# Kernel tuning notes

Hardware: AMD Instinct MI355X
Metric: run time of the kernel (lower is better)

Reference implementation:

```python
import jax, jax.numpy as jnp
import numpy as np

N_NODES = 50000
N_FEAT = 32
HIDDEN = 64
K_HOPS = 3
N_EDGES = 800000
BN_EPS = 1e-5


def setup_inputs() -> dict:
    key = jax.random.key(0)
    ks = jax.random.split(key, 16)
    x = jax.random.normal(ks[0], (N_NODES, N_FEAT), jnp.float32)
    edge_index = jax.random.randint(ks[1], (2, N_EDGES), 0, N_NODES, jnp.int32)
    edge_weight = jax.random.uniform(ks[2], (N_EDGES,), jnp.float32, minval=0.1, maxval=1.0)
    fin = N_FEAT + HIDDEN  # DCRNN cell concatenates [X, H]
    s = 1.0 / np.sqrt(fin)
    Wz = jax.random.uniform(ks[3], (2, K_HOPS, fin, HIDDEN), jnp.float32, -s, s)
    Wr = jax.random.uniform(ks[4], (2, K_HOPS, fin, HIDDEN), jnp.float32, -s, s)
    Wh = jax.random.uniform(ks[5], (2, K_HOPS, fin, HIDDEN), jnp.float32, -s, s)
    bz = jax.random.uniform(ks[6], (HIDDEN,), jnp.float32, -s, s)
    br = jax.random.uniform(ks[7], (HIDDEN,), jnp.float32, -s, s)
    bh = jax.random.uniform(ks[8], (HIDDEN,), jnp.float32, -s, s)
    g = 1.0 / np.sqrt(HIDDEN)
    gcn_w = jax.random.uniform(ks[9], (HIDDEN, HIDDEN), jnp.float32, -g, g)
    gcn_b = jax.random.uniform(ks[10], (HIDDEN,), jnp.float32, -g, g)
    bn_gamma = jnp.ones((HIDDEN,), jnp.float32)
    bn_beta = jnp.zeros((HIDDEN,), jnp.float32)
    lin_w = jax.random.uniform(ks[11], (HIDDEN, 1), jnp.float32, -g, g)
    lin_b = jax.random.uniform(ks[12], (1,), jnp.float32, -g, g)
    return dict(x=x, edge_index=edge_index, edge_weight=edge_weight,
                Wz=Wz, bz=bz, Wr=Wr, br=br, Wh=Wh, bh=bh,
                gcn_w=gcn_w, gcn_b=gcn_b, bn_gamma=bn_gamma, bn_beta=bn_beta,
                lin_w=lin_w, lin_b=lin_b)


def _dconv(X, W, b, row, col, ew, do_inv, di_inv, n):
    # Diffusion conv: H = sum_k T_out^k(X) @ W[0,k] + T_in^k(X) @ W[1,k] + b
    # T_out: propagate along edges (source -> target), out-degree normalized
    # T_in : propagate along reversed edges, in-degree normalized
    H = X @ W[0, 0] + X @ W[1, 0]
    Tx_o = X
    Tx_i = X
    w_out = (ew * do_inv[row])[:, None]  # [E,1]
    w_in = (ew * di_inv[col])[:, None]   # [E,1]
    for k in range(1, W.shape[1]):
        Tx_o = jax.ops.segment_sum(w_out * Tx_o[row], col, num_segments=n)
        Tx_i = jax.ops.segment_sum(w_in * Tx_i[col], row, num_segments=n)
        H = H + Tx_o @ W[0, k] + Tx_i @ W[1, k]
    return H + b


def reference(x, edge_index, edge_weight, Wz, bz, Wr, br, Wh, bh,
              gcn_w, gcn_b, bn_gamma, bn_beta, lin_w, lin_b):
    n = x.shape[0]
    row, col = edge_index[0], edge_index[1]
    # weighted degrees (as in DConv's dense-adjacency degree computation)
    deg_out = jax.ops.segment_sum(edge_weight, row, num_segments=n)
    deg_in = jax.ops.segment_sum(edge_weight, col, num_segments=n)
    do_inv = jnp.where(deg_out > 0, 1.0 / deg_out, 0.0)
    di_inv = jnp.where(deg_in > 0, 1.0 / deg_in, 0.0)

    # --- DCRNN cell (GRU with diffusion convs), hidden state starts at zero ---
    H0 = jnp.zeros((n, Wz.shape[-1]), x.dtype)
    XH = jnp.concatenate([x, H0], axis=1)
    Z = jax.nn.sigmoid(_dconv(XH, Wz, bz, row, col, edge_weight, do_inv, di_inv, n))
    R = jax.nn.sigmoid(_dconv(XH, Wr, br, row, col, edge_weight, do_inv, di_inv, n))
    XHR = jnp.concatenate([x, H0 * R], axis=1)
    H_tilde = jnp.tanh(_dconv(XHR, Wh, bh, row, col, edge_weight, do_inv, di_inv, n))
    H = Z * H0 + (1.0 - Z) * H_tilde  # [N, HIDDEN]

    # --- GCNConv(H, edge_index) with unit edge weights + self loops, sym norm ---
    xw = H @ gcn_w
    ones_e = jnp.ones((row.shape[0],), x.dtype)
    deg = jax.ops.segment_sum(ones_e, col, num_segments=n) + 1.0  # + self loop
    dis = jnp.where(deg > 0, jax.lax.rsqrt(deg), 0.0)
    norm = (dis[row] * dis[col])[:, None]
    y = jax.ops.segment_sum(norm * xw[row], col, num_segments=n) + (dis * dis)[:, None] * xw
    y = y + gcn_b

    # ReLU -> BatchNorm1d (batch statistics, biased var) -> Dropout(identity/eval) -> Linear
    y = jax.nn.relu(y)
    mean = jnp.mean(y, axis=0)
    var = jnp.mean(jnp.square(y - mean), axis=0)
    y = (y - mean) * jax.lax.rsqrt(var + BN_EPS) * bn_gamma + bn_beta
    out = y @ lin_w + lin_b  # [N, 1]
    return out
```

## Files before the change

### kernel.cpp

```cpp
#include <hip/hip_runtime.h>
#include <hip/hip_fp16.h>
#include <math.h>


#define BN_EPS 1e-5f
#define CAPB 6
#define CAP  64
#define ITEMS 2048
#define KI 8
#define REGCAP 5120

typedef _Float16 v8h __attribute__((ext_vector_type(8)));
typedef float v4f __attribute__((ext_vector_type(4)));

__global__ __launch_bounds__(256) void k_sort1(
    const int* __restrict__ row, const int* __restrict__ col,
    const float* __restrict__ ew,
    unsigned long long* __restrict__ bufC, unsigned long long* __restrict__ bufR,
    unsigned* __restrict__ gcnt, int E, int nbk, int reg) {
    __shared__ unsigned hist[256], scanb[256], cur[256], runb[256];
    __shared__ unsigned long long outb[ITEMS];
    int t = threadIdx.x;
    int s = (blockIdx.x >= nbk) ? 1 : 0;
    int blk = blockIdx.x - s * nbk;
    int e0 = blk * ITEMS;
    int vcnt = E - e0; if (vcnt > ITEMS) vcnt = ITEMS;
    hist[t] = 0;
    __syncthreads();
    for (int k = 0; k < KI; ++k) {
        int e = e0 + k * 256 + t;
        if (e < E) {
            int key = s ? row[e] : col[e];
            atomicAdd(&hist[key >> 8], 1u);
        }
    }
    __syncthreads();
    scanb[t] = hist[t];
    __syncthreads();
    for (int off = 1; off < 256; off <<= 1) {
        unsigned v = (t >= off) ? scanb[t - off] : 0u;
        __syncthreads();
        scanb[t] += v;
        __syncthreads();
    }
    unsigned excl = scanb[t] - hist[t];
    __syncthreads();
    scanb[t] = excl;
    cur[t] = excl;
    runb[t] = (unsigned)(t * reg) + atomicAdd(&gcnt[s * 256 + t], hist[t]);
    __syncthreads();
    for (int k = 0; k < KI; ++k) {
        int e = e0 + k * 256 + t;
        if (e < E) {
            int key, oth;
            if (s) { key = row[e]; oth = col[e]; }
            else   { key = col[e]; oth = row[e]; }
            unsigned hw = (unsigned)__half_as_ushort(__float2half(ew[e]));
            unsigned long long it = ((unsigned long long)(unsigned)key << 32)
                                  | ((unsigned)oth << 16) | hw;
            unsigned r = atomicAdd(&cur[key >> 8], 1u);
            outb[r] = it;
        }
    }
    __syncthreads();
    unsigned long long* buf = s ? bufR : bufC;
    for (int k = 0; k < KI; ++k) {
        int idx = k * 256 + t;
        if (idx < vcnt) {
            unsigned long long it = outb[idx];
            unsigned d = (unsigned)(it >> 40) & 255u;
            buf[(size_t)runb[d] + ((unsigned)idx - scanb[d])] = it;
        }
    }
}

__device__ inline float ent_w(unsigned e) {
    return __half2float(__ushort_as_half((unsigned short)(e & 0xffffu)));
}

__global__ __launch_bounds__(256) void k_sort2(
    const unsigned long long* __restrict__ bufC, const unsigned long long* __restrict__ bufR,
    const unsigned* __restrict__ gcnt,
    unsigned* __restrict__ ent_col, unsigned* __restrict__ ent_row,
    int* __restrict__ cnt_col, int* __restrict__ cnt_row,
    float* __restrict__ di_inv, float* __restrict__ do_inv, float* __restrict__ dis,
    int N, int reg, int ndig) {
    __shared__ unsigned hist[256], scanb[256], cur[256];
    __shared__ unsigned outp[REGCAP];
    __shared__ unsigned char outl[REGCAP];
    int t = threadIdx.x;
    int s = (blockIdx.x >= ndig) ? 1 : 0;
    int d0 = blockIdx.x - s * ndig;
    const unsigned long long* src = (s ? bufR : bufC) + (size_t)d0 * reg;
    unsigned* ent = s ? ent_row : ent_col;
    int cin = (int)gcnt[s * 256 + d0]; if (cin > REGCAP) cin = REGCAP;
    hist[t] = 0;
    __syncthreads();
    for (int i = t; i < cin; i += 256) {
        unsigned l = (unsigned)(src[i] >> 32) & 255u;
        atomicAdd(&hist[l], 1u);
    }
    __syncthreads();
    scanb[t] = hist[t];
    __syncthreads();
    for (int off = 1; off < 256; off <<= 1) {
        unsigned v = (t >= off) ? scanb[t - off] : 0u;
        __syncthreads();
        scanb[t] += v;
        __syncthreads();
    }
    unsigned excl = scanb[t] - hist[t];
    __syncthreads();
    scanb[t] = excl;
    cur[t] = excl;
    __syncthreads();
    for (int i = t; i < cin; i += 256) {
        unsigned long long it = src[i];
        unsigned l = (unsigned)(it >> 32) & 255u;
        unsigned r = atomicAdd(&cur[l], 1u);
        outp[r] = (unsigned)it;
        outl[r] = (unsigned char)l;
    }
    __syncthreads();
    int node0 = d0 << 8;
    for (int i = t; i < cin; i += 256) {
        unsigned l = outl[i];
        int slot = i - (int)scanb[l];
        int node = node0 + (int)l;
        if (slot < CAP && node < N)
            ent[((size_t)node << CAPB) + slot] = outp[i];
    }
    int node = node0 + t;
    if (node < N) {
        unsigned beg = scanb[t], n = hist[t];
        float sum = 0.f;
        for (unsigned j = 0; j < n; ++j) sum += ent_w(outp[beg + j]);
        float inv = sum > 0.f ? 1.f / sum : 0.f;
        if (s) { do_inv[node] = inv; cnt_row[node] = (int)n; }
        else   { di_inv[node] = inv; cnt_col[node] = (int)n;
                 dis[node] = rsqrtf((float)n + 1.0f); }
    }
}

__global__ void k_cvt_x(const float* __restrict__ xf, __half* __restrict__ xh, int n2) {
    int t = blockIdx.x * blockDim.x + threadIdx.x;
    if (t >= n2) return;
    float2 v = *(const float2*)(xf + 2 * (size_t)t);
    __half2 h; h.x = __float2half(v.x); h.y = __float2half(v.y);
    *(__half2*)(xh + 2 * (size_t)t) = h;
}

__global__ void k_hop(const unsigned* __restrict__ ent_col, const unsigned* __restrict__ ent_row,
                      const int* __restrict__ cnt_col, const int* __restrict__ cnt_row,
                      const __half* __restrict__ So, const __half* __restrict__ Si,
                      const float* __restrict__ do_inv, const float* __restrict__ di_inv,
                      __half* __restrict__ Do, __half* __restrict__ Di, int N) {
    int t = blockIdx.x * blockDim.x + threadIdx.x;
    int f = t & 31;
    int p = t >> 5;
    if (p >= 2 * N) return;
    const unsigned* ent; const __half* S; const float* inv; __half* D;
    int d, cnt;
    if (p < N) { d = p;     ent = ent_col; S = So; inv = do_inv; D = Do; cnt = min(cnt_col[d], CAP); }
    else       { d = p - N; ent = ent_row; S = Si; inv = di_inv; D = Di; cnt = min(cnt_row[d], CAP); }
    ent += ((size_t)d << CAPB);
    float acc = 0.f;
    int j = 0;
    for (; j + 7 < cnt; j += 8) {
        unsigned e0 = ent[j],     e1 = ent[j + 1], e2 = ent[j + 2], e3 = ent[j + 3];
        unsigned e4 = ent[j + 4], e5 = ent[j + 5], e6 = ent[j + 6], e7 = ent[j + 7];
        int s0 = e0 >> 16, s1 = e1 >> 16, s2 = e2 >> 16, s3 = e3 >> 16;
        int s4 = e4 >> 16, s5 = e5 >> 16, s6 = e6 >> 16, s7 = e7 >> 16;
        float i0 = inv[s0], i1 = inv[s1], i2 = inv[s2], i3 = inv[s3];
        float i4 = inv[s4], i5 = inv[s5], i6 = inv[s6], i7 = inv[s7];
        float v0 = __half2float(S[(size_t)s0 * 32 + f]);
        float v1 = __half2float(S[(size_t)s1 * 32 + f]);
        float v2 = __half2float(S[(size_t)s2 * 32 + f]);
        float v3 = __half2float(S[(size_t)s3 * 32 + f]);
        float v4 = __half2float(S[(size_t)s4 * 32 + f]);
        float v5 = __half2float(S[(size_t)s5 * 32 + f]);
        float v6 = __half2float(S[(size_t)s6 * 32 + f]);
        float v7 = __half2float(S[(size_t)s7 * 32 + f]);
        acc += ent_w(e0) * i0 * v0 + ent_w(e1) * i1 * v1
             + ent_w(e2) * i2 * v2 + ent_w(e3) * i3 * v3
             + ent_w(e4) * i4 * v4 + ent_w(e5) * i5 * v5
             + ent_w(e6) * i6 * v6 + ent_w(e7) * i7 * v7;
    }
    for (; j + 3 < cnt; j += 4) {
        unsigned e0 = ent[j],     e1 = ent[j + 1];
        unsigned e2 = ent[j + 2], e3 = ent[j + 3];
        int s0 = e0 >> 16, s1 = e1 >> 16, s2 = e2 >> 16, s3 = e3 >> 16;
        float i0 = inv[s0], i1 = inv[s1], i2 = inv[s2], i3 = inv[s3];
        float v0 = __half2float(S[(size_t)s0 * 32 + f]);
        float v1 = __half2float(S[(size_t)s1 * 32 + f]);
        float v2 = __half2float(S[(size_t)s2 * 32 + f]);
        float v3 = __half2float(S[(size_t)s3 * 32 + f]);
        acc += ent_w(e0) * i0 * v0 + ent_w(e1) * i1 * v1
             + ent_w(e2) * i2 * v2 + ent_w(e3) * i3 * v3;
    }
    for (; j < cnt; ++j) {
        unsigned e0 = ent[j];
        int s0 = e0 >> 16;
        acc += ent_w(e0) * inv[s0] * __half2float(S[(size_t)s0 * 32 + f]);
    }
    D[(size_t)d * 32 + f] = __float2half(acc);
}

__global__ void k_wprep(const float* __restrict__ Wz, const float* __restrict__ Wh,
                        const float* __restrict__ gcn_w,
                        __half* __restrict__ wzT, __half* __restrict__ whT,
                        __half* __restrict__ gwT) {
    int t = blockIdx.x * blockDim.x + threadIdx.x;
    if (t < 64 * 160) {
        int c = t / 160, k = t % 160;
        int blk = k >> 5, r = k & 31;
        float vz, vh;
        if (blk == 0) {
            vz = Wz[r * 64 + c] + Wz[(288 + r) * 64 + c];
            vh = Wh[r * 64 + c] + Wh[(288 + r) * 64 + c];
        } else {
            int kk = (blk + 1) >> 1, dd = (blk + 1) & 1;
            int off = ((dd * 3 + kk) * 96 + r) * 64 + c;
            vz = Wz[off]; vh = Wh[off];
        }
        wzT[t] = __float2half(vz);
        whT[t] = __float2half(vh);
    }
    if (t < 64 * 64) {
        int c = t >> 6, k = t & 63;
        gwT[t] = __float2half(gcn_w[k * 64 + c]);
    }
}

__device__ inline v8h ldh8(const __half* p) { return *(const v8h*)p; }

__global__ __launch_bounds__(256) void k_zh_mfma(
    const __half* __restrict__ xh, const __half* __restrict__ t1o,
    const __half* __restrict__ t1i, const __half* __restrict__ t2o,
    const __half* __restrict__ t2i,
    const __half* __restrict__ wzT, const __half* __restrict__ whT,
    const float* __restrict__ bz, const float* __restrict__ bh,
    const float* __restrict__ dis, __half* __restrict__ Hd, int N) {
    int lane = threadIdx.x & 63;
    int wv = threadIdx.x >> 6;
    int q = lane >> 4, m = lane & 15;
    int c = wv * 16 + m;
    int ko = q * 8;

    const __half* wz = wzT + c * 160 + ko;
    const __half* wh = whT + c * 160 + ko;
    v8h bz0 = ldh8(wz),       bh0 = ldh8(wh);
    v8h bz1 = ldh8(wz + 32),  bh1 = ldh8(wh + 32);
    v8h bz2 = ldh8(wz + 64),  bh2 = ldh8(wh + 64);
    v8h bz3 = ldh8(wz + 96),  bh3 = ldh8(wh + 96);
    v8h bz4 = ldh8(wz + 128), bh4 = ldh8(wh + 128);
    float bzc = bz[c], bhc = bh[c];

    int T = (N + 15) >> 4;
    for (int t = blockIdx.x; t < T; t += gridDim.x) {
        int n0 = t << 4;
        int nn = n0 + m; if (nn > N - 1) nn = N - 1;
        size_t off = (size_t)nn * 32 + ko;
        v8h a0 = ldh8(xh + off);
        v8h a1 = ldh8(t1o + off);
        v8h a2 = ldh8(t1i + off);
        v8h a3 = ldh8(t2o + off);
        v8h a4 = ldh8(t2i + off);
        v4f az = {0.f, 0.f, 0.f, 0.f}, ah = {0.f, 0.f, 0.f, 0.f};
        az = __builtin_amdgcn_mfma_f32_16x16x32_f16(a0, bz0, az, 0, 0, 0);
        ah = __builtin_amdgcn_mfma_f32_16x16x32_f16(a0, bh0, ah, 0, 0, 0);
        az = __builtin_amdgcn_mfma_f32_16x16x32_f16(a1, bz1, az, 0, 0, 0);
        ah = __builtin_amdgcn_mfma_f32_16x16x32_f16(a1, bh1, ah, 0, 0, 0);
        az = __builtin_amdgcn_mfma_f32_16x16x32_f16(a2, bz2, az, 0, 0, 0);
        ah = __builtin_amdgcn_mfma_f32_16x16x32_f16(a2, bh2, ah, 0, 0, 0);
        az = __builtin_amdgcn_mfma_f32_16x16x32_f16(a3, bz3, az, 0, 0, 0);
        ah = __builtin_amdgcn_mfma_f32_16x16x32_f16(a3, bh3, ah, 0, 0, 0);
        az = __builtin_amdgcn_mfma_f32_16x16x32_f16(a4, bz4, az, 0, 0, 0);
        ah = __builtin_amdgcn_mfma_f32_16x16x32_f16(a4, bh4, ah, 0, 0, 0);

#pragma unroll
        for (int i = 0; i < 4; ++i) {
            float zv = 1.f / (1.f + expf(-(az[i] + bzc)));
            float hv = (1.f - zv) * tanhf(ah[i] + bhc);
            int node = n0 + q * 4 + i;
            if (node < N) Hd[(size_t)node * 64 + c] = __float2half(dis[node] * hv);
        }
    }
}

__global__ __launch_bounds__(256) void k_agg(
    const unsigned* __restrict__ ent_col, const int* __restrict__ cnt_col,
    const float* __restrict__ dis, const __half* __restrict__ Hd,
    __half* __restrict__ P, int N) {
    int t = blockIdx.x * blockDim.x + threadIdx.x;
    int ch = t & 63;
    int d = t >> 6;
    if (d >= N) return;
    const unsigned* ent = ent_col + ((size_t)d << CAPB);
    int cnt = min(cnt_col[d], CAP);
    float acc = __half2float(Hd[(size_t)d * 64 + ch]);
    int j = 0;
    for (; j + 7 < cnt; j += 8) {
        unsigned e0 = ent[j],     e1 = ent[j + 1], e2 = ent[j + 2], e3 = ent[j + 3];
        unsigned e4 = ent[j + 4], e5 = ent[j + 5], e6 = ent[j + 6], e7 = ent[j + 7];
        float v0 = __half2float(Hd[(size_t)(e0 >> 16) * 64 + ch]);
        float v1 = __half2float(Hd[(size_t)(e1 >> 16) * 64 + ch]);
        float v2 = __half2float(Hd[(size_t)(e2 >> 16) * 64 + ch]);
        float v3 = __half2float(Hd[(size_t)(e3 >> 16) * 64 + ch]);
        float v4 = __half2float(Hd[(size_t)(e4 >> 16) * 64 + ch]);
        float v5 = __half2float(Hd[(size_t)(e5 >> 16) * 64 + ch]);
        float v6 = __half2float(Hd[(size_t)(e6 >> 16) * 64 + ch]);
        float v7 = __half2float(Hd[(size_t)(e7 >> 16) * 64 + ch]);
        acc += (v0 + v1 + v2 + v3) + (v4 + v5 + v6 + v7);
    }
    for (; j + 3 < cnt; j += 4) {
        unsigned e0 = ent[j],     e1 = ent[j + 1];
        unsigned e2 = ent[j + 2], e3 = ent[j + 3];
        float v0 = __half2float(Hd[(size_t)(e0 >> 16) * 64 + ch]);
        float v1 = __half2float(Hd[(size_t)(e1 >> 16) * 64 + ch]);
        float v2 = __half2float(Hd[(size_t)(e2 >> 16) * 64 + ch]);
        float v3 = __half2float(Hd[(size_t)(e3 >> 16) * 64 + ch]);
        acc += v0 + v1 + v2 + v3;
    }
    for (; j < cnt; ++j) {
        acc += __half2float(Hd[(size_t)(ent[j] >> 16) * 64 + ch]);
    }
    P[(size_t)d * 64 + ch] = __float2half(dis[d] * acc);
}

__global__ __launch_bounds__(256) void k_gcn2(
    const __half* __restrict__ P, const __half* __restrict__ gwT,
    const float* __restrict__ gcn_b,
    float* __restrict__ y, float* __restrict__ stats, int N) {
    __shared__ float red[2][256];
    int lane = threadIdx.x & 63;
    int wv = threadIdx.x >> 6;
    int q = lane >> 4, m = lane & 15;
    int c = wv * 16 + m;
    int ko = q * 8;
    v8h g0 = ldh8(gwT + c * 64 + ko);
    v8h g1 = ldh8(gwT + c * 64 + 32 + ko);
    float bl = gcn_b[c];
    float sa = 0.f, s2a = 0.f;
    int T = (N + 15) >> 4;
    for (int t = blockIdx.x; t < T; t += gridDim.x) {
        int n0 = t << 4;
        int nn = n0 + m; if (nn > N - 1) nn = N - 1;
        const __half* pr = P + (size_t)nn * 64;
        v8h a0 = ldh8(pr + ko);
        v8h a1 = ldh8(pr + 32 + ko);
        v4f acc = {0.f, 0.f, 0.f, 0.f};
        acc = __builtin_amdgcn_mfma_f32_16x16x32_f16(a0, g0, acc, 0, 0, 0);
        acc = __builtin_amdgcn_mfma_f32_16x16x32_f16(a1, g1, acc, 0, 0, 0);
#pragma unroll
        for (int i = 0; i < 4; ++i) {
            int node = n0 + q * 4 + i;
            if (node < N) {
                float v = acc[i] + bl;
                v = v > 0.f ? v : 0.f;
                y[(size_t)node * 64 + c] = v;
                sa += v; s2a += v * v;
            }
        }
    }
    red[0][threadIdx.x] = sa;
    red[1][threadIdx.x] = s2a;
    __syncthreads();
    if (q == 0) {
        int t0 = threadIdx.x;
        float ts  = red[0][t0] + red[0][t0 + 16] + red[0][t0 + 32] + red[0][t0 + 48];
        float ts2 = red[1][t0] + red[1][t0 + 16] + red[1][t0 + 32] + red[1][t0 + 48];
        atomicAdd(&stats[c], ts);
        atomicAdd(&stats[64 + c], ts2);
    }
}

__global__ void k_final(const float* __restrict__ y, const float* __restrict__ stats,
                        const float* __restrict__ gma, const float* __restrict__ bta,
                        const float* __restrict__ lw, const float* __restrict__ lb,
                        float* __restrict__ out, int N) {
    int lane = threadIdx.x & 63;
    int wave = (blockIdx.x * blockDim.x + threadIdx.x) >> 6;
    if (wave >= N) return;
    float invN = 1.0f / (float)N;
    float mean = stats[lane] * invN;
    float var  = stats[64 + lane] * invN - mean * mean;
    float istd = rsqrtf(var + BN_EPS);
    float v = y[(size_t)wave * 64 + lane];
    float t = (v - mean) * istd * gma[lane] + bta[lane];
    float p = t * lw[lane];
    for (int off = 32; off > 0; off >>= 1)
        p += __shfl_down(p, off, 64);
    if (lane == 0) out[wave] = p + lb[0];
}

extern "C" void kernel_launch(void* const* d_in, const int* in_sizes, int n_in,
                              void* d_out, int out_size, void* d_ws, size_t ws_size,
                              hipStream_t stream) {
    const float* x     = (const float*)d_in[0];
    const int*   ei    = (const int*)d_in[1];
    const float* ew    = (const float*)d_in[2];
    const float* Wz    = (const float*)d_in[3];
    const float* bz    = (const float*)d_in[4];
    const float* Wh    = (const float*)d_in[7];
    const float* bhv   = (const float*)d_in[8];
    const float* gcn_w = (const float*)d_in[9];
    const float* gcn_b = (const float*)d_in[10];
    const float* gma   = (const float*)d_in[11];
    const float* bta   = (const float*)d_in[12];
    const float* lw    = (const float*)d_in[13];
    const float* lb    = (const float*)d_in[14];
    float* out = (float*)d_out;

    const int N = in_sizes[0] / 32;
    const int E = in_sizes[2];
    const int* row = ei;
    const int* col = ei + E;

    float* ws      = (float*)d_ws;
    int*   cnt_col = (int*)ws;
    int*   cnt_row = (int*)(ws + (size_t)N);
    unsigned* gcnt = (unsigned*)(ws + 2 * (size_t)N);
    float* stats   = ws + 2 * (size_t)N + 512;
    size_t Z0      = 2 * (size_t)N + 640;
    float* dis     = ws + Z0;
    float* do_inv  = ws + Z0 + (size_t)N;
    float* di_inv  = ws + Z0 + 2 * (size_t)N;
    __half* xh     = (__half*)(ws + Z0 + 3 * (size_t)N);
    __half* txo1   = (__half*)(ws + Z0 + 19 * (size_t)N);
    __half* txi1   = (__half*)(ws + Z0 + 35 * (size_t)N);
    __half* txo2   = (__half*)(ws + Z0 + 51 * (size_t)N);
    __half* txi2   = (__half*)(ws + Z0 + 67 * (size_t)N);
    unsigned* ent_col = (unsigned*)(ws + Z0 + 83 * (size_t)N);
    unsigned* ent_row = ent_col + ((size_t)N << CAPB);
    __half* wzT    = (__half*)(ws + Z0 + 211 * (size_t)N);
    __half* whT    = wzT + 64 * 160;
    __half* gwT    = whT + 64 * 160;
    unsigned long long* bufC = (unsigned long long*)(ws + Z0 + 211 * (size_t)N + 16384);
    unsigned long long* bufR = bufC + (size_t)256 * REGCAP;

    __half* Hd = (__half*)ent_row;
    __half* P  = (__half*)xh;
    float*  yb = (float*)ent_col;

    hipMemsetAsync((char*)d_ws + 2 * (size_t)N * sizeof(float), 0,
                   640 * sizeof(float), stream);

    int nbk = (E + ITEMS - 1) / ITEMS;
    int ndig = (N + 255) / 256;
    k_cvt_x<<<(16 * N + 255) / 256, 256, 0, stream>>>(x, xh, 16 * N);
    k_wprep<<<40, 256, 0, stream>>>(Wz, Wh, gcn_w, wzT, whT, gwT);
    k_sort1<<<2 * nbk, 256, 0, stream>>>(row, col, ew, bufC, bufR, gcnt, E, nbk, REGCAP);
    k_sort2<<<2 * ndig, 256, 0, stream>>>(bufC, bufR, gcnt, ent_col, ent_row,
                                          cnt_col, cnt_row, di_inv, do_inv, dis,
                                          N, REGCAP, ndig);

    int bhop = (2 * N * 32 + 255) / 256;
    k_hop<<<bhop, 256, 0, stream>>>(ent_col, ent_row, cnt_col, cnt_row,
                                    xh, xh, do_inv, di_inv, txo1, txi1, N);
    k_hop<<<bhop, 256, 0, stream>>>(ent_col, ent_row, cnt_col, cnt_row,
                                    txo1, txi1, do_inv, di_inv, txo2, txi2, N);

    k_zh_mfma<<<1024, 256, 0, stream>>>(xh, txo1, txi1, txo2, txi2,
                                        wzT, whT, bz, bhv, dis, Hd, N);

    k_agg<<<(64 * N + 255) / 256, 256, 0, stream>>>(ent_col, cnt_col, dis, Hd, P, N);
    k_gcn2<<<1024, 256, 0, stream>>>(P, gwT, gcn_b, yb, stats, N);
    k_final<<<(N + 3) / 4, 256, 0, stream>>>(yb, stats, gma, bta, lw, lb, out, N);
}
```

Baseline: 276.3 us.

## Fuse GCN aggregation into MFMA GEMM kernel and vectorize hop gathers to half2

The diffusion hop kernel now has each thread handle two features through half2 loads, so half as many threads issue the index and weight loads per node. The separate GCN neighbor-aggregation kernel is merged into the MFMA GEMM kernel. Each 16-node tile is aggregated into shared memory and then fed straight to MFMA, which removes the P buffer round trip and one launch. The fused kernel runs a fixed 1024-block grid with extra block syncs, which may lower the parallelism available for the gather-heavy aggregation.

New measurement: 268.8 us. 2.7% less time.

```diff
diff --git a/kernel.cpp b/kernel.cpp
--- a/kernel.cpp
+++ b/kernel.cpp
@@ -152,58 +152,64 @@
 
 __global__ void k_hop(const unsigned* __restrict__ ent_col, const unsigned* __restrict__ ent_row,
                       const int* __restrict__ cnt_col, const int* __restrict__ cnt_row,
-                      const __half* __restrict__ So, const __half* __restrict__ Si,
+                      const __half2* __restrict__ So, const __half2* __restrict__ Si,
                       const float* __restrict__ do_inv, const float* __restrict__ di_inv,
-                      __half* __restrict__ Do, __half* __restrict__ Di, int N) {
+                      __half2* __restrict__ Do, __half2* __restrict__ Di, int N) {
     int t = blockIdx.x * blockDim.x + threadIdx.x;
-    int f = t & 31;
-    int p = t >> 5;
+    int f = t & 15;
+    int p = t >> 4;
     if (p >= 2 * N) return;
-    const unsigned* ent; const __half* S; const float* inv; __half* D;
+    const unsigned* ent; const __half2* S; const float* inv; __half2* D;
     int d, cnt;
     if (p < N) { d = p;     ent = ent_col; S = So; inv = do_inv; D = Do; cnt = min(cnt_col[d], CAP); }
     else       { d = p - N; ent = ent_row; S = Si; inv = di_inv; D = Di; cnt = min(cnt_row[d], CAP); }
     ent += ((size_t)d << CAPB);
-    float acc = 0.f;
+    float a0 = 0.f, a1 = 0.f;
     int j = 0;
     for (; j + 7 < cnt; j += 8) {
         unsigned e0 = ent[j],     e1 = ent[j + 1], e2 = ent[j + 2], e3 = ent[j + 3];
         unsigned e4 = ent[j + 4], e5 = ent[j + 5], e6 = ent[j + 6], e7 = ent[j + 7];
         int s0 = e0 >> 16, s1 = e1 >> 16, s2 = e2 >> 16, s3 = e3 >> 16;
         int s4 = e4 >> 16, s5 = e5 >> 16, s6 = e6 >> 16, s7 = e7 >> 16;
-        float i0 = inv[s0], i1 = inv[s1], i2 = inv[s2], i3 = inv[s3];
-        float i4 = inv[s4], i5 = inv[s5], i6 = inv[s6], i7 = inv[s7];
-        float v0 = __half2float(S[(size_t)s0 * 32 + f]);
-        float v1 = __half2float(S[(size_t)s1 * 32 + f]);
-        float v2 = __half2float(S[(size_t)s2 * 32 + f]);
-        float v3 = __half2float(S[(size_t)s3 * 32 + f]);
-        float v4 = __half2float(S[(size_t)s4 * 32 + f]);
-        float v5 = __half2float(S[(size_t)s5 * 32 + f]);
-        float v6 = __half2float(S[(size_t)s6 * 32 + f]);
-        float v7 = __half2float(S[(size_t)s7 * 32 + f]);
-        acc += ent_w(e0) * i0 * v0 + ent_w(e1) * i1 * v1
-             + ent_w(e2) * i2 * v2 + ent_w(e3) * i3 * v3
-             + ent_w(e4) * i4 * v4 + ent_w(e5) * i5 * v5
-             + ent_w(e6) * i6 * v6 + ent_w(e7) * i7 * v7;
+        float w0 = ent_w(e0) * inv[s0], w1 = ent_w(e1) * inv[s1];
+        float w2 = ent_w(e2) * inv[s2], w3 = ent_w(e3) * inv[s3];
+        float w4 = ent_w(e4) * inv[s4], w5 = ent_w(e5) * inv[s5];
+        float w6 = ent_w(e6) * inv[s6], w7 = ent_w(e7) * inv[s7];
+        float2 v0 = __half22float2(S[(size_t)s0 * 16 + f]);
+        float2 v1 = __half22float2(S[(size_t)s1 * 16 + f]);
+        float2 v2 = __half22float2(S[(size_t)s2 * 16 + f]);
+        float2 v3 = __half22float2(S[(size_t)s3 * 16 + f]);
+        float2 v4 = __half22float2(S[(size_t)s4 * 16 + f]);
+        float2 v5 = __half22float2(S[(size_t)s5 * 16 + f]);
+        float2 v6 = __half22float2(S[(size_t)s6 * 16 + f]);
+        float2 v7 = __half22float2(S[(size_t)s7 * 16 + f]);
+        a0 += w0 * v0.x + w1 * v1.x + w2 * v2.x + w3 * v3.x
+            + w4 * v4.x + w5 * v5.x + w6 * v6.x + w7 * v7.x;
+        a1 += w0 * v0.y + w1 * v1.y + w2 * v2.y + w3 * v3.y
+            + w4 * v4.y + w5 * v5.y + w6 * v6.y + w7 * v7.y;
     }
     for (; j + 3 < cnt; j += 4) {
         unsigned e0 = ent[j],     e1 = ent[j + 1];
         unsigned e2 = ent[j + 2], e3 = ent[j + 3];
         int s0 = e0 >> 16, s1 = e1 >> 16, s2 = e2 >> 16, s3 = e3 >> 16;
-        float i0 = inv[s0], i1 = inv[s1], i2 = inv[s2], i3 = inv[s3];
-        float v0 = __half2float(S[(size_t)s0 * 32 + f]);
-        float v1 = __half2float(S[(size_t)s1 * 32 + f]);
-        float v2 = __half2float(S[(size_t)s2 * 32 + f]);
-        float v3 = __half2float(S[(size_t)s3 * 32 + f]);
-        acc += ent_w(e0) * i0 * v0 + ent_w(e1) * i1 * v1
-             + ent_w(e2) * i2 * v2 + ent_w(e3) * i3 * v3;
+        float w0 = ent_w(e0) * inv[s0], w1 = ent_w(e1) * inv[s1];
+        float w2 = ent_w(e2) * inv[s2], w3 = ent_w(e3) * inv[s3];
+        float2 v0 = __half22float2(S[(size_t)s0 * 16 + f]);
+        float2 v1 = __half22float2(S[(size_t)s1 * 16 + f]);
+        float2 v2 = __half22float2(S[(size_t)s2 * 16 + f]);
+        float2 v3 = __half22float2(S[(size_t)s3 * 16 + f]);
+        a0 += w0 * v0.x + w1 * v1.x + w2 * v2.x + w3 * v3.x;
+        a1 += w0 * v0.y + w1 * v1.y + w2 * v2.y + w3 * v3.y;
     }
     for (; j < cnt; ++j) {
         unsigned e0 = ent[j];
         int s0 = e0 >> 16;
-        acc += ent_w(e0) * inv[s0] * __half2float(S[(size_t)s0 * 32 + f]);
-    }
-    D[(size_t)d * 32 + f] = __float2half(acc);
+        float w0 = ent_w(e0) * inv[s0];
+        float2 v0 = __half22float2(S[(size_t)s0 * 16 + f]);
+        a0 += w0 * v0.x;
+        a1 += w0 * v0.y;
+    }
+    D[(size_t)d * 16 + f] = __floats2half2_rn(a0, a1);
 }
 
 __global__ void k_wprep(const float* __restrict__ Wz, const float* __restrict__ Wh,
@@ -288,50 +294,12 @@
     }
 }
 
-__global__ __launch_bounds__(256) void k_agg(
+__global__ __launch_bounds__(256) void k_aggw(
     const unsigned* __restrict__ ent_col, const int* __restrict__ cnt_col,
     const float* __restrict__ dis, const __half* __restrict__ Hd,
-    __half* __restrict__ P, int N) {
-    int t = blockIdx.x * blockDim.x + threadIdx.x;
-    int ch = t & 63;
-    int d = t >> 6;
-    if (d >= N) return;
-    const unsigned* ent = ent_col + ((size_t)d << CAPB);
-    int cnt = min(cnt_col[d], CAP);
-    float acc = __half2float(Hd[(size_t)d * 64 + ch]);
-    int j = 0;
-    for (; j + 7 < cnt; j += 8) {
-        unsigned e0 = ent[j],     e1 = ent[j + 1], e2 = ent[j + 2], e3 = ent[j + 3];
-        unsigned e4 = ent[j + 4], e5 = ent[j + 5], e6 = ent[j + 6], e7 = ent[j + 7];
-        float v0 = __half2float(Hd[(size_t)(e0 >> 16) * 64 + ch]);
-        float v1 = __half2float(Hd[(size_t)(e1 >> 16) * 64 + ch]);
-        float v2 = __half2float(Hd[(size_t)(e2 >> 16) * 64 + ch]);
-        float v3 = __half2float(Hd[(size_t)(e3 >> 16) * 64 + ch]);
-        float v4 = __half2float(Hd[(size_t)(e4 >> 16) * 64 + ch]);
-        float v5 = __half2float(Hd[(size_t)(e5 >> 16) * 64 + ch]);
-        float v6 = __half2float(Hd[(size_t)(e6 >> 16) * 64 + ch]);
-        float v7 = __half2float(Hd[(size_t)(e7 >> 16) * 64 + ch]);
-        acc += (v0 + v1 + v2 + v3) + (v4 + v5 + v6 + v7);
-    }
-    for (; j + 3 < cnt; j += 4) {
-        unsigned e0 = ent[j],     e1 = ent[j + 1];
-        unsigned e2 = ent[j + 2], e3 = ent[j + 3];
-        float v0 = __half2float(Hd[(size_t)(e0 >> 16) * 64 + ch]);
-        float v1 = __half2float(Hd[(size_t)(e1 >> 16) * 64 + ch]);
-        float v2 = __half2float(Hd[(size_t)(e2 >> 16) * 64 + ch]);
-        float v3 = __half2float(Hd[(size_t)(e3 >> 16) * 64 + ch]);
-        acc += v0 + v1 + v2 + v3;
-    }
-    for (; j < cnt; ++j) {
-        acc += __half2float(Hd[(size_t)(ent[j] >> 16) * 64 + ch]);
-    }
-    P[(size_t)d * 64 + ch] = __float2half(dis[d] * acc);
-}
-
-__global__ __launch_bounds__(256) void k_gcn2(
-    const __half* __restrict__ P, const __half* __restrict__ gwT,
-    const float* __restrict__ gcn_b,
+    const __half* __restrict__ gwT, const float* __restrict__ gcn_b,
     float* __restrict__ y, float* __restrict__ stats, int N) {
+    __shared__ _Float16 Hl[16 * 72];
     __shared__ float red[2][256];
     int lane = threadIdx.x & 63;
     int wv = threadIdx.x >> 6;
@@ -345,10 +313,46 @@
     int T = (N + 15) >> 4;
     for (int t = blockIdx.x; t < T; t += gridDim.x) {
         int n0 = t << 4;
-        int nn = n0 + m; if (nn > N - 1) nn = N - 1;
-        const __half* pr = P + (size_t)nn * 64;
-        v8h a0 = ldh8(pr + ko);
-        v8h a1 = ldh8(pr + 32 + ko);
+#pragma unroll
+        for (int i = 0; i < 4; ++i) {
+            int d = n0 + wv * 4 + i;
+            float acc = 0.f;
+            if (d < N) {
+                acc = __half2float(Hd[(size_t)d * 64 + lane]);
+                const unsigned* ent = ent_col + ((size_t)d << CAPB);
+                int cnt = min(cnt_col[d], CAP);
+                int j = 0;
+                for (; j + 7 < cnt; j += 8) {
+                    unsigned e0 = ent[j],     e1 = ent[j + 1], e2 = ent[j + 2], e3 = ent[j + 3];
+                    unsigned e4 = ent[j + 4], e5 = ent[j + 5], e6 = ent[j + 6], e7 = ent[j + 7];
+                    float v0 = __half2float(Hd[(size_t)(e0 >> 16) * 64 + lane]);
+                    float v1 = __half2float(Hd[(size_t)(e1 >> 16) * 64 + lane]);
+                    float v2 = __half2float(Hd[(size_t)(e2 >> 16) * 64 + lane]);
+                    float v3 = __half2float(Hd[(size_t)(e3 >> 16) * 64 + lane]);
+                    float v4 = __half2float(Hd[(size_t)(e4 >> 16) * 64 + lane]);
+                    float v5 = __half2float(Hd[(size_t)(e5 >> 16) * 64 + lane]);
+                    float v6 = __half2float(Hd[(size_t)(e6 >> 16) * 64 + lane]);
+                    float v7 = __half2float(Hd[(size_t)(e7 >> 16) * 64 + lane]);
+                    acc += (v0 + v1 + v2 + v3) + (v4 + v5 + v6 + v7);
+                }
+                for (; j + 3 < cnt; j += 4) {
+                    unsigned e0 = ent[j],     e1 = ent[j + 1];
+                    unsigned e2 = ent[j + 2], e3 = ent[j + 3];
+                    float v0 = __half2float(Hd[(size_t)(e0 >> 16) * 64 + lane]);
+                    float v1 = __half2float(Hd[(size_t)(e1 >> 16) * 64 + lane]);
+                    float v2 = __half2float(Hd[(size_t)(e2 >> 16) * 64 + lane]);
+                    float v3 = __half2float(Hd[(size_t)(e3 >> 16) * 64 + lane]);
+                    acc += v0 + v1 + v2 + v3;
+                }
+                for (; j < cnt; ++j)
+                    acc += __half2float(Hd[(size_t)(ent[j] >> 16) * 64 + lane]);
+                acc *= dis[d];
+            }
+            Hl[(wv * 4 + i) * 72 + lane] = (_Float16)acc;
+        }
+        __syncthreads();
+        v8h a0 = *(const v8h*)&Hl[m * 72 + ko];
+        v8h a1 = *(const v8h*)&Hl[m * 72 + 32 + ko];
         v4f acc = {0.f, 0.f, 0.f, 0.f};
         acc = __builtin_amdgcn_mfma_f32_16x16x32_f16(a0, g0, acc, 0, 0, 0);
         acc = __builtin_amdgcn_mfma_f32_16x16x32_f16(a1, g1, acc, 0, 0, 0);
@@ -362,6 +366,7 @@
                 sa += v; s2a += v * v;
             }
         }
+        __syncthreads();
     }
     red[0][threadIdx.x] = sa;
     red[1][threadIdx.x] = s2a;
@@ -440,8 +445,7 @@
     unsigned long long* bufR = bufC + (size_t)256 * REGCAP;
 
     __half* Hd = (__half*)ent_row;
-    __half* P  = (__half*)xh;
-    float*  yb = (float*)ent_col;
+    float*  yb = (float*)txo1;
 
     hipMemsetAsync((char*)d_ws + 2 * (size_t)N * sizeof(float), 0,
                    640 * sizeof(float), stream);
@@ -455,16 +459,20 @@
                                           cnt_col, cnt_row, di_inv, do_inv, dis,
                                           N, REGCAP, ndig);
 
-    int bhop = (2 * N * 32 + 255) / 256;
+    int bhop = (2 * N * 16 + 255) / 256;
     k_hop<<<bhop, 256, 0, stream>>>(ent_col, ent_row, cnt_col, cnt_row,
-                                    xh, xh, do_inv, di_inv, txo1, txi1, N);
+                                    (const __half2*)xh, (const __half2*)xh,
+                                    do_inv, di_inv,
+                                    (__half2*)txo1, (__half2*)txi1, N);
     k_hop<<<bhop, 256, 0, stream>>>(ent_col, ent_row, cnt_col, cnt_row,
-                                    txo1, txi1, do_inv, di_inv, txo2, txi2, N);
+                                    (const __half2*)txo1, (const __half2*)txi1,
+                                    do_inv, di_inv,
+                                    (__half2*)txo2, (__half2*)txi2, N);
 
     k_zh_mfma<<<1024, 256, 0, stream>>>(xh, txo1, txi1, txo2, txi2,
                                         wzT, whT, bz, bhv, dis, Hd, N);
 
-    k_agg<<<(64 * N + 255) / 256, 256, 0, stream>>>(ent_col, cnt_col, dis, Hd, P, N);
-    k_gcn2<<<1024, 256, 0, stream>>>(P, gwT, gcn_b, yb, stats, N);
+    k_aggw<<<1024, 256, 0, stream>>>(ent_col, cnt_col, dis, Hd, gwT, gcn_b,
+                                     yb, stats, N);
     k_final<<<(N + 3) / 4, 256, 0, stream>>>(yb, stats, gma, bta, lw, lb, out, N);
 }
```
